# Kernel optimization log

Hardware: AMD Instinct MI355X
Metric: run time of the kernel (lower is better)

## Reference

```python
import jax, jax.numpy as jnp
import numpy as np

N = 50000      # total nodes (cells + row/col/caption nodes across the batch of tables)
E = 500000     # graph edges (row/col cliques, extra edges)
P = 131072     # candidate edge pairs for the edge head
D_LM = 768     # bert-base hidden size
D_MF = 64      # max_freq_emb_size
H = 4          # num_heads per GAT layer
D = 128        # hidden_layer_size per head
DIN = D_LM + D_MF  # 832
DOUT = H * D       # 512


def setup_inputs() -> dict:
    key = jax.random.key(0)
    ks = jax.random.split(key, 32)
    r = lambda k, sh, s=1.0: jax.random.normal(k, sh, jnp.float32) * s
    inp = {}
    inp['cell_h'] = r(ks[0], (N, D_LM))
    inp['pos_emb'] = r(ks[1], (4, D_LM), 0.02)
    inp['mf_emb'] = r(ks[2], (6, D_MF), 0.02)
    # GAT layer 1 (in 832 -> 4 heads x 128), no residual
    inp['W1'] = r(ks[3], (DIN, DOUT), DIN ** -0.5)
    inp['al1'] = r(ks[4], (H, D), D ** -0.5)
    inp['ar1'] = r(ks[5], (H, D), D ** -0.5)
    inp['b1'] = jnp.zeros((DOUT,), jnp.float32)
    # GAT layer 2 (512 -> 4 heads x 128), identity residual
    inp['W2'] = r(ks[6], (DOUT, DOUT), DOUT ** -0.5)
    inp['al2'] = r(ks[7], (H, D), D ** -0.5)
    inp['ar2'] = r(ks[8], (H, D), D ** -0.5)
    inp['b2'] = jnp.zeros((DOUT,), jnp.float32)
    # comp_and_gid head: Linear(512,256)+BN+ReLU+Linear(256,4)
    inp['Wg1'] = r(ks[9], (DOUT, 256), DOUT ** -0.5)
    inp['bg1'] = jnp.zeros((256,), jnp.float32)
    inp['g_gamma'] = jnp.ones((256,), jnp.float32)
    inp['g_beta'] = jnp.zeros((256,), jnp.float32)
    inp['g_mean'] = jnp.zeros((256,), jnp.float32)
    inp['g_var'] = jnp.ones((256,), jnp.float32)
    inp['Wg2'] = r(ks[10], (256, 4), 256 ** -0.5)
    inp['bg2'] = jnp.zeros((4,), jnp.float32)
    # edge head: Linear(1024,256)+BN+ReLU+Linear(256,1)
    inp['We1'] = r(ks[11], (2 * DOUT, 256), (2 * DOUT) ** -0.5)
    inp['be1'] = jnp.zeros((256,), jnp.float32)
    inp['e_gamma'] = jnp.ones((256,), jnp.float32)
    inp['e_beta'] = jnp.zeros((256,), jnp.float32)
    inp['e_mean'] = jnp.zeros((256,), jnp.float32)
    inp['e_var'] = jnp.ones((256,), jnp.float32)
    inp['We2'] = r(ks[12], (256, 1), 256 ** -0.5)
    inp['be2'] = jnp.zeros((1,), jnp.float32)
    # graph structure / index features (constants)
    inp['src'] = jax.random.randint(ks[13], (E,), 0, N, jnp.int32)
    inp['dst'] = jax.random.randint(ks[14], (E,), 0, N, jnp.int32)
    inp['row_pos'] = jax.random.randint(ks[15], (N,), 0, 4, jnp.int32)
    inp['col_pos'] = jax.random.randint(ks[16], (N,), 0, 4, jnp.int32)
    inp['row_mf'] = jax.random.randint(ks[17], (N,), 0, 6, jnp.int32)
    inp['col_mf'] = jax.random.randint(ks[18], (N,), 0, 6, jnp.int32)
    inp['pairs'] = jax.random.randint(ks[19], (P, 2), 0, N, jnp.int32)
    return inp


def _gat(h, W, al, ar, b, src, dst, residual):
    """DGL-style GATConv: LeakyReLU(a_l.Wh_src + a_r.Wh_dst), edge-softmax over dst."""
    n = h.shape[0]
    feat = (h @ W).reshape(n, H, D)                     # [N,H,D]
    el = jnp.sum(feat * al, axis=-1)                    # [N,H]
    er = jnp.sum(feat * ar, axis=-1)                    # [N,H]
    e = jax.nn.leaky_relu(el[src] + er[dst], 0.2)       # [E,H]
    emax = jax.ops.segment_max(e, dst, num_segments=n)  # per-dst max (stability)
    ee = jnp.exp(e - emax[dst])
    denom = jax.ops.segment_sum(ee, dst, num_segments=n)
    alpha = ee / denom[dst]                             # [E,H]
    out = jax.ops.segment_sum(feat[src] * alpha[:, :, None], dst, num_segments=n)  # [N,H,D]
    if residual:
        out = out + h.reshape(n, H, D)                  # identity residual (in==H*D)
    return (out + b.reshape(H, D)).reshape(n, H * D)


def _bn(x, gamma, beta, mean, var):
    return (x - mean) * jax.lax.rsqrt(var + 1e-5) * gamma + beta


def reference(cell_h, pos_emb, mf_emb, W1, al1, ar1, b1, W2, al2, ar2, b2,
              Wg1, bg1, g_gamma, g_beta, g_mean, g_var, Wg2, bg2,
              We1, be1, e_gamma, e_beta, e_mean, e_var, We2, be2,
              src, dst, row_pos, col_pos, row_mf, col_mf, pairs):
    # embedding fusion: LM cell embeddings + row/col positional embeddings
    h = cell_h + pos_emb[row_pos] + pos_emb[col_pos]                    # [N,768]
    mf = mf_emb[jnp.minimum(row_mf, 5)] + mf_emb[jnp.minimum(col_mf, 5)]  # [N,64]
    h = jnp.concatenate([h, mf], axis=-1)                               # [N,832]
    # two multi-head GATConv layers (dropout inactive at eval)
    h = _gat(h, W1, al1, ar1, b1, src, dst, residual=False)             # [N,512]
    h = _gat(h, W2, al2, ar2, b2, src, dst, residual=True)              # [N,512]
    # comp_and_gid head
    gid_logits = jax.nn.relu(_bn(h @ Wg1 + bg1, g_gamma, g_beta, g_mean, g_var)) @ Wg2 + bg2  # [N,4]
    # edge head over candidate node pairs
    ef = jnp.concatenate([h[pairs[:, 0]], h[pairs[:, 1]]], axis=-1)     # [P,1024]
    edge_logits = jax.nn.relu(_bn(ef @ We1 + be1, e_gamma, e_beta, e_mean, e_var)) @ We2 + be2  # [P,1]
    return gid_logits, edge_logits
```

## Files before the change

### kernel.cpp

```cpp
#include <hip/hip_runtime.h>
#include <math.h>


typedef __attribute__((ext_vector_type(8))) short short8;
typedef __attribute__((ext_vector_type(4))) float f32x4;
typedef unsigned short ushort;

#define GLOAD16(g, l)                                                   \
  __builtin_amdgcn_global_load_lds(                                     \
      (const __attribute__((address_space(1))) unsigned int*)(g),       \
      (__attribute__((address_space(3))) unsigned int*)(l), 16, 0, 0)

__device__ __forceinline__ float b2f(ushort h) {
  union { unsigned u; float f; } v; v.u = ((unsigned)h) << 16; return v.f;
}
__device__ __forceinline__ ushort f2b(float f) {
  union { float f; unsigned u; } v; v.f = f;
  unsigned r = v.u + 0x7fffu + ((v.u >> 16) & 1u);
  return (ushort)(r >> 16);
}
__device__ __forceinline__ void up4(uint2 q, float* o) {
  o[0] = b2f((ushort)(q.x & 0xffffu)); o[1] = b2f((ushort)(q.x >> 16));
  o[2] = b2f((ushort)(q.y & 0xffffu)); o[3] = b2f((ushort)(q.y >> 16));
}
__device__ __forceinline__ void up8(uint4 q, float* o) {
  o[0] = b2f((ushort)(q.x & 0xffffu)); o[1] = b2f((ushort)(q.x >> 16));
  o[2] = b2f((ushort)(q.y & 0xffffu)); o[3] = b2f((ushort)(q.y >> 16));
  o[4] = b2f((ushort)(q.z & 0xffffu)); o[5] = b2f((ushort)(q.z >> 16));
  o[6] = b2f((ushort)(q.w & 0xffffu)); o[7] = b2f((ushort)(q.w >> 16));
}
__device__ __forceinline__ uint4 pk8(const float* o) {
  uint4 q;
  q.x = (unsigned)f2b(o[0]) | ((unsigned)f2b(o[1]) << 16);
  q.y = (unsigned)f2b(o[2]) | ((unsigned)f2b(o[3]) << 16);
  q.z = (unsigned)f2b(o[4]) | ((unsigned)f2b(o[5]) << 16);
  q.w = (unsigned)f2b(o[6]) | ((unsigned)f2b(o[7]) << 16);
  return q;
}
__device__ __forceinline__ float warp_sum(float v) {
#pragma unroll
  for (int o = 32; o > 0; o >>= 1) v += __shfl_xor(v, o);
  return v;
}

__global__ __launch_bounds__(256) void embed_kernel(
    const float* __restrict__ cell_h, const float* __restrict__ pos_emb,
    const float* __restrict__ mf_emb,
    const int* __restrict__ row_pos, const int* __restrict__ col_pos,
    const int* __restrict__ row_mf, const int* __restrict__ col_mf,
    ushort* __restrict__ X0, int N)
{
  const int idx = blockIdx.x * 256 + threadIdx.x;
  const int total = N * 104;
  if (idx >= total) return;
  const int n = idx / 104;
  const int c8 = (idx - n * 104) * 8;
  float o[8];
  if (c8 < 768) {
    const int rp = row_pos[n], cp = col_pos[n];
    const float4* pc = (const float4*)(cell_h + (size_t)n * 768 + c8);
    const float4* pr = (const float4*)(pos_emb + (size_t)rp * 768 + c8);
    const float4* pq = (const float4*)(pos_emb + (size_t)cp * 768 + c8);
    float4 c0 = pc[0], c1 = pc[1], r0 = pr[0], r1 = pr[1], q0 = pq[0], q1 = pq[1];
    o[0] = c0.x + r0.x + q0.x; o[1] = c0.y + r0.y + q0.y;
    o[2] = c0.z + r0.z + q0.z; o[3] = c0.w + r0.w + q0.w;
    o[4] = c1.x + r1.x + q1.x; o[5] = c1.y + r1.y + q1.y;
    o[6] = c1.z + r1.z + q1.z; o[7] = c1.w + r1.w + q1.w;
  } else {
    const int rm = min(row_mf[n], 5), cm = min(col_mf[n], 5);
    const int j0 = c8 - 768;
    const float4* pr = (const float4*)(mf_emb + (size_t)rm * 64 + j0);
    const float4* pq = (const float4*)(mf_emb + (size_t)cm * 64 + j0);
    float4 r0 = pr[0], r1 = pr[1], q0 = pq[0], q1 = pq[1];
    o[0] = r0.x + q0.x; o[1] = r0.y + q0.y; o[2] = r0.z + q0.z; o[3] = r0.w + q0.w;
    o[4] = r1.x + q1.x; o[5] = r1.y + q1.y; o[6] = r1.z + q1.z; o[7] = r1.w + q1.w;
  }
  *(uint4*)(X0 + (size_t)n * 832 + c8) = pk8(o);
}

__global__ __launch_bounds__(256) void wpack_kernel(
    const float* __restrict__ W, ushort* __restrict__ Wp,
    int K, int srcN, int colBase, int nTK)
{
  const int idx = blockIdx.x * 256 + threadIdx.x;
  if (idx >= K * srcN) return;
  const int c = idx / K, k = idx - c * K;
  const int n = colBase + c;
  const int tn = n >> 7, tk = k >> 6;
  const int sub = (((n >> 4) & 7) << 1) | ((k >> 5) & 1);
  const int lane = (n & 15) | (((k >> 3) & 3) << 4);
  const int j = k & 7;
  const size_t off = (((size_t)(tn * nTK + tk) << 4) + sub) * 512 + lane * 8 + j;
  Wp[off] = f2b(W[(size_t)k * srcN + c]);
}

__global__ void eprep_kernel(const float* __restrict__ be1,
                             const float* __restrict__ eg, const float* __restrict__ eb,
                             const float* __restrict__ em, const float* __restrict__ ev,
                             float* __restrict__ sa_ext, float* __restrict__ sb)
{
  const int c = threadIdx.x;
  const float sa = eg[c] * rsqrtf(ev[c] + 1e-5f);
  sa_ext[c] = sa;
  sa_ext[c + 256] = sa;
  sb[c] = eb[c] + (be1[c] - em[c]) * sa;
}

template <int EPI, bool ELR>
__global__ __launch_bounds__(256) void mfma_gemm_kernel(
    const ushort* __restrict__ A, const ushort* __restrict__ Bp,
    ushort* __restrict__ C0, ushort* __restrict__ C1,
    int M, int K, int Ncols, int NT, int mtiles,
    const float* __restrict__ bias, const float* __restrict__ gamma,
    const float* __restrict__ beta, const float* __restrict__ mean,
    const float* __restrict__ var, const float* __restrict__ sa_ext,
    const float* __restrict__ al, const float* __restrict__ ar,
    float* __restrict__ elp, float* __restrict__ erp)
{
  __shared__ ushort LDS[16896];
  __shared__ float redS[256];
  ushort* As = LDS;
  ushort* Bs = LDS + 8192;
  const int tid = threadIdx.x;
  const int lane = tid & 63;
  const int wave = tid >> 6;
  const int wm = wave >> 1, wn = wave & 1;

  const int per = NT << 3;
  const int f = blockIdx.x;
  const int sg = f / per;
  const int rem = f - sg * per;
  const int nb = min(8, mtiles - (sg << 3));
  const int band = rem % nb, colt = rem / nb;
  const int m0 = ((sg << 3) + band) << 7;
  const int n0 = colt << 7;
  const int nTK = K >> 6;

  const int rA = lane & 15;
  const int kA = (lane >> 4) << 3;
  const ushort* Aaddr[4];
#pragma unroll
  for (int q = 0; q < 4; ++q) {
    const int a = (wave << 2) + q;
    int row = m0 + ((a >> 1) << 4) + rA;
    if (row >= M) row = 0;
    Aaddr[q] = A + (size_t)row * K + ((a & 1) << 5) + kA;
  }
  const ushort* Baddr = Bp + (((size_t)colt * nTK) << 13)
                        + ((size_t)(wave << 2) << 9) + (lane << 3);

  f32x4 acc[4][4];
#pragma unroll
  for (int i = 0; i < 4; ++i)
#pragma unroll
    for (int j = 0; j < 4; ++j) acc[i][j] = (f32x4){0.f, 0.f, 0.f, 0.f};

  for (int k0 = 0; k0 < K; k0 += 64) {
    __syncthreads();
#pragma unroll
    for (int q = 0; q < 4; ++q)
      GLOAD16(Aaddr[q] + k0, As + (((wave << 2) + q) << 9));
#pragma unroll
    for (int q = 0; q < 4; ++q)
      GLOAD16(Baddr + (((size_t)(k0 >> 6)) << 13) + (q << 9),
              Bs + (((wave << 2) + q) << 9));
    __syncthreads();
#pragma unroll
    for (int ks = 0; ks < 2; ++ks) {
      short8 af[4], bf4[4];
#pragma unroll
      for (int x = 0; x < 4; ++x)
        af[x] = *(const short8*)(As + ((((wm << 2) + x) * 2 + ks) << 9) + (lane << 3));
#pragma unroll
      for (int x = 0; x < 4; ++x)
        bf4[x] = *(const short8*)(Bs + ((((wn << 2) + x) * 2 + ks) << 9) + (lane << 3));
#pragma unroll
      for (int mf = 0; mf < 4; ++mf)
#pragma unroll
        for (int nf = 0; nf < 4; ++nf)
          acc[mf][nf] = __builtin_amdgcn_mfma_f32_16x16x32_bf16(
              af[mf], bf4[nf], acc[mf][nf], 0, 0, 0);
    }
  }

  __syncthreads();
#pragma unroll
  for (int nf = 0; nf < 4; ++nf) {
    const int cl = (((wn << 2) + nf) << 4) + (lane & 15);
    const int col = n0 + cl;
    float sa = 1.f, sb = 0.f;
    bool dorelu = false;
    if (EPI == 1) {
      if (col < 256) {
        const float rs = rsqrtf(var[col] + 1e-5f);
        sa = rs * gamma[col];
        sb = beta[col] + (bias[col] - mean[col]) * sa;
        dorelu = true;
      } else {
        sa = sa_ext[col - 256];
      }
    }
#pragma unroll
    for (int mf = 0; mf < 4; ++mf) {
      const int rl = (((wm << 2) + mf) << 4) + ((lane >> 4) << 2);
#pragma unroll
      for (int j = 0; j < 4; ++j) {
        float v = acc[mf][nf][j];
        if (EPI == 1) { v = fmaf(v, sa, sb); if (dorelu) v = fmaxf(v, 0.f); }
        LDS[(rl + j) * 132 + cl] = f2b(v);
      }
    }
  }
  __syncthreads();
#pragma unroll
  for (int i = 0; i < 8; ++i) {
    const int g = tid + (i << 8);
    const int r = g >> 4, c8 = g & 15;
    const int row = m0 + r;
    if (row >= M) continue;
    const uint4 v = *(const uint4*)(LDS + r * 132 + (c8 << 3));
    const int col = n0 + (c8 << 3);
    if (EPI == 0) {
      *(uint4*)(C0 + (size_t)row * Ncols + col) = v;
    } else {
      if (col < 256) *(uint4*)(C0 + (size_t)row * 256 + col) = v;
      else           *(uint4*)(C1 + (size_t)row * 512 + (col - 256)) = v;
    }
  }

  if (ELR) {
    const int r = tid & 127;
    const int half = tid >> 7;
    const float* alh = al + colt * 128 + half * 64;
    const float* arh = ar + colt * 128 + half * 64;
    const ushort* rowp = LDS + r * 132 + half * 64;
    float sl = 0.f, sr = 0.f;
#pragma unroll
    for (int c = 0; c < 64; ++c) {
      const float v = b2f(rowp[c]);
      sl = fmaf(v, alh[c], sl);
      sr = fmaf(v, arh[c], sr);
    }
    if (half) { redS[r] = sl; redS[r + 128] = sr; }
    __syncthreads();
    if (!half) {
      const int row = m0 + r;
      if (row < M) {
        elp[(size_t)row * 4 + colt] = sl + redS[r];
        erp[(size_t)row * 4 + colt] = sr + redS[r + 128];
      }
    }
  }
}

__global__ __launch_bounds__(256) void hist_kernel(
    const int* __restrict__ dst, int* __restrict__ counts, int E)
{
  const int e = blockIdx.x * 256 + threadIdx.x;
  if (e < E) atomicAdd(counts + dst[e], 1);
}

__global__ __launch_bounds__(1024) void scan_kernel(
    const int* __restrict__ counts, int* __restrict__ offsets, int N)
{
  __shared__ int sums[1024];
  const int t = threadIdx.x;
  const int chunk = (N + 1023) >> 10;
  const int beg = t * chunk;
  const int end = min(beg + chunk, N);
  int s = 0;
  for (int i = beg; i < end; ++i) s += counts[i];
  sums[t] = s;
  __syncthreads();
  for (int o = 1; o < 1024; o <<= 1) {
    int u = (t >= o) ? sums[t - o] : 0;
    __syncthreads();
    sums[t] += u;
    __syncthreads();
  }
  int run = sums[t] - s;
  for (int i = beg; i < end; ++i) { offsets[i] = run; run += counts[i]; }
  if (t == 1023) offsets[N] = sums[1023];
}

__global__ __launch_bounds__(256) void scatter_kernel(
    const int* __restrict__ src, const int* __restrict__ dst,
    const int* __restrict__ offsets, int* __restrict__ cursor,
    int* __restrict__ csr_src, int E)
{
  const int e = blockIdx.x * 256 + threadIdx.x;
  if (e >= E) return;
  const int d = dst[e];
  const int pos = offsets[d] + atomicAdd(cursor + d, 1);
  csr_src[pos] = src[e];
}

template <bool RES>
__global__ __launch_bounds__(256) void gat_aggregate_kernel(
    const int* __restrict__ csr_src, const int* __restrict__ offsets,
    const float* __restrict__ el, const float* __restrict__ er,
    const ushort* __restrict__ feat, const float* __restrict__ bias,
    const ushort* __restrict__ resid, ushort* __restrict__ out, int N)
{
  __shared__ float eeS[4][1024];
  __shared__ int sS[4][256];
  const int w = threadIdx.x >> 6;
  const int node = (blockIdx.x * 256 + threadIdx.x) >> 6;
  const int lane = threadIdx.x & 63;
  if (node >= N) return;
  const int beg = offsets[node], end = offsets[node + 1];
  const int deg = end - beg;
  const float4 erd = *(const float4*)(er + (size_t)node * 4);
  float* eew = eeS[w];
  int* sw = sS[w];

  float d0 = 0.f, d1 = 0.f, d2 = 0.f, d3 = 0.f;
  for (int i = lane; i < deg; i += 64) {
    const int s = csr_src[beg + i];
    const float4 l = *(const float4*)(el + (size_t)s * 4);
    float x0 = l.x + erd.x, x1 = l.y + erd.y, x2 = l.z + erd.z, x3 = l.w + erd.w;
    x0 = x0 > 0.f ? x0 : 0.2f * x0;
    x1 = x1 > 0.f ? x1 : 0.2f * x1;
    x2 = x2 > 0.f ? x2 : 0.2f * x2;
    x3 = x3 > 0.f ? x3 : 0.2f * x3;
    const float e0 = __expf(x0), e1 = __expf(x1), e2 = __expf(x2), e3 = __expf(x3);
    if (i < 256) {
      float4 ev = {e0, e1, e2, e3};
      *(float4*)(eew + (i << 2)) = ev;
      sw[i] = s;
    }
    d0 += e0; d1 += e1; d2 += e2; d3 += e3;
  }
  d0 = warp_sum(d0); d1 = warp_sum(d1); d2 = warp_sum(d2); d3 = warp_sum(d3);
  const float r0 = 1.f / d0, r1 = 1.f / d1, r2 = 1.f / d2, r3 = 1.f / d3;
  const int h = lane >> 4;
  const float rh = (lane & 32) ? ((lane & 16) ? r3 : r2) : ((lane & 16) ? r1 : r0);
  const float erh = (lane & 32) ? ((lane & 16) ? erd.w : erd.z)
                                : ((lane & 16) ? erd.y : erd.x);

  float a[8] = {0.f, 0.f, 0.f, 0.f, 0.f, 0.f, 0.f, 0.f};
  for (int i = 0; i < deg; ++i) {
    int s;
    float ew;
    if (i < 256) {
      s = sw[i];
      ew = eew[(i << 2) | h];
    } else {
      s = csr_src[beg + i];
      float x = el[(size_t)s * 4 + h] + erh;
      x = x > 0.f ? x : 0.2f * x;
      ew = __expf(x);
    }
    const float aw = ew * rh;
    const uint4 q = *(const uint4*)(feat + (size_t)s * 512 + lane * 8);
    float v[8];
    up8(q, v);
#pragma unroll
    for (int j = 0; j < 8; ++j) a[j] = fmaf(v[j], aw, a[j]);
  }

  const float4 b0 = *(const float4*)(bias + lane * 8);
  const float4 b1 = *(const float4*)(bias + lane * 8 + 4);
  a[0] += b0.x; a[1] += b0.y; a[2] += b0.z; a[3] += b0.w;
  a[4] += b1.x; a[5] += b1.y; a[6] += b1.z; a[7] += b1.w;
  if (RES) {
    float q[8];
    up8(*(const uint4*)(resid + (size_t)node * 512 + lane * 8), q);
#pragma unroll
    for (int j = 0; j < 8; ++j) a[j] += q[j];
  }
  *(uint4*)(out + (size_t)node * 512 + lane * 8) = pk8(a);
}

__global__ __launch_bounds__(256) void gid2_kernel(
    const ushort* __restrict__ g, const float* __restrict__ Wg2,
    const float* __restrict__ bg2, float* __restrict__ out, int N)
{
  const int wv = (blockIdx.x * 256 + threadIdx.x) >> 6;
  const int lane = threadIdx.x & 63;
  if (wv >= N) return;
  float ga[4];
  up4(*(const uint2*)(g + (size_t)wv * 256 + lane * 4), ga);
  float a0 = 0.f, a1 = 0.f, a2 = 0.f, a3 = 0.f;
  const float* wp = Wg2 + (size_t)lane * 16;
#pragma unroll
  for (int j = 0; j < 4; j++) {
    const float4 w = *(const float4*)(wp + j * 4);
    a0 += ga[j] * w.x; a1 += ga[j] * w.y; a2 += ga[j] * w.z; a3 += ga[j] * w.w;
  }
  a0 = warp_sum(a0); a1 = warp_sum(a1); a2 = warp_sum(a2); a3 = warp_sum(a3);
  if (lane == 0) {
    float4 o = {a0 + bg2[0], a1 + bg2[1], a2 + bg2[2], a3 + bg2[3]};
    *(float4*)(out + (size_t)wv * 4) = o;
  }
}

__global__ __launch_bounds__(256) void pair_combine_kernel(
    const ushort* __restrict__ UV, const int* __restrict__ pairs,
    const float* __restrict__ sb, const float* __restrict__ We2,
    const float* __restrict__ be2, float* __restrict__ out, int P)
{
  const int hw = (blockIdx.x * 256 + threadIdx.x) >> 5;
  const int l = threadIdx.x & 31;
  if (hw >= P) return;
  const int p0 = pairs[2 * hw], p1 = pairs[2 * hw + 1];
  float u[8], v[8];
  up8(*(const uint4*)(UV + (size_t)p0 * 512 + l * 8), u);
  up8(*(const uint4*)(UV + (size_t)p1 * 512 + 256 + l * 8), v);
  const float4 sb0 = *(const float4*)(sb + l * 8);
  const float4 sb1 = *(const float4*)(sb + l * 8 + 4);
  const float4 w0 = *(const float4*)(We2 + l * 8);
  const float4 w1 = *(const float4*)(We2 + l * 8 + 4);
  float s = fmaxf(u[0] + v[0] + sb0.x, 0.f) * w0.x
          + fmaxf(u[1] + v[1] + sb0.y, 0.f) * w0.y
          + fmaxf(u[2] + v[2] + sb0.z, 0.f) * w0.z
          + fmaxf(u[3] + v[3] + sb0.w, 0.f) * w0.w
          + fmaxf(u[4] + v[4] + sb1.x, 0.f) * w1.x
          + fmaxf(u[5] + v[5] + sb1.y, 0.f) * w1.y
          + fmaxf(u[6] + v[6] + sb1.z, 0.f) * w1.z
          + fmaxf(u[7] + v[7] + sb1.w, 0.f) * w1.w;
#pragma unroll
  for (int o = 16; o > 0; o >>= 1) s += __shfl_xor(s, o);
  if (l == 0) out[hw] = s + be2[0];
}

extern "C" void kernel_launch(void* const* d_in, const int* in_sizes, int n_in,
                              void* d_out, int out_size, void* d_ws, size_t ws_size,
                              hipStream_t stream) {
  const float* cell_h  = (const float*)d_in[0];
  const float* pos_emb = (const float*)d_in[1];
  const float* mf_emb  = (const float*)d_in[2];
  const float* W1  = (const float*)d_in[3];
  const float* al1 = (const float*)d_in[4];
  const float* ar1 = (const float*)d_in[5];
  const float* b1  = (const float*)d_in[6];
  const float* W2  = (const float*)d_in[7];
  const float* al2 = (const float*)d_in[8];
  const float* ar2 = (const float*)d_in[9];
  const float* b2  = (const float*)d_in[10];
  const float* Wg1 = (const float*)d_in[11];
  const float* bg1 = (const float*)d_in[12];
  const float* g_gamma = (const float*)d_in[13];
  const float* g_beta  = (const float*)d_in[14];
  const float* g_mean  = (const float*)d_in[15];
  const float* g_var   = (const float*)d_in[16];
  const float* Wg2 = (const float*)d_in[17];
  const float* bg2 = (const float*)d_in[18];
  const float* We1 = (const float*)d_in[19];
  const float* be1 = (const float*)d_in[20];
  const float* e_gamma = (const float*)d_in[21];
  const float* e_beta  = (const float*)d_in[22];
  const float* e_mean  = (const float*)d_in[23];
  const float* e_var   = (const float*)d_in[24];
  const float* We2 = (const float*)d_in[25];
  const float* be2 = (const float*)d_in[26];
  const int* src = (const int*)d_in[27];
  const int* dst = (const int*)d_in[28];
  const int* row_pos = (const int*)d_in[29];
  const int* col_pos = (const int*)d_in[30];
  const int* row_mf  = (const int*)d_in[31];
  const int* col_mf  = (const int*)d_in[32];
  const int* pairs   = (const int*)d_in[33];

  const int N = in_sizes[0] / 768;
  const int E = in_sizes[27];
  const int P = in_sizes[33] / 2;

  ushort* X0    = (ushort*)d_ws;
  ushort* featB = X0 + (size_t)N * 832;
  ushort* h1    = featB + (size_t)N * 512;
  ushort* h2    = h1 + (size_t)N * 512;
  ushort* W1p   = h2 + (size_t)N * 512;
  ushort* W2p   = W1p + 512 * 832;
  ushort* Bh    = W2p + 512 * 512;
  float* sa_ext = (float*)(Bh + 768 * 512);
  float* sbv    = sa_ext + 512;
  float* el     = sbv + 256;
  float* er     = el + (size_t)N * 4;
  int* offsets  = (int*)(er + (size_t)N * 4);
  int* counts   = offsets + (N + 1);
  int* csr_src  = counts + N;
  ushort* g_tmp = X0;
  ushort* UV    = featB;

  const int nodeWaves = (N + 3) / 4;
  const int mtiles = (N + 127) / 128;

  hipMemsetAsync(counts, 0, (size_t)N * sizeof(int), stream);
  hist_kernel<<<(E + 255) / 256, 256, 0, stream>>>(dst, counts, E);
  scan_kernel<<<1, 1024, 0, stream>>>(counts, offsets, N);
  hipMemsetAsync(counts, 0, (size_t)N * sizeof(int), stream);
  scatter_kernel<<<(E + 255) / 256, 256, 0, stream>>>(src, dst, offsets, counts, csr_src, E);

  wpack_kernel<<<(512 * 832 + 255) / 256, 256, 0, stream>>>(W1, W1p, 832, 512, 0, 13);
  wpack_kernel<<<(512 * 512 + 255) / 256, 256, 0, stream>>>(W2, W2p, 512, 512, 0, 8);
  wpack_kernel<<<(512 * 256 + 255) / 256, 256, 0, stream>>>(Wg1, Bh, 512, 256, 0, 8);
  wpack_kernel<<<(512 * 256 + 255) / 256, 256, 0, stream>>>(We1, Bh, 512, 256, 256, 8);
  wpack_kernel<<<(512 * 256 + 255) / 256, 256, 0, stream>>>(We1 + 512 * 256, Bh, 512, 256, 512, 8);
  eprep_kernel<<<1, 256, 0, stream>>>(be1, e_gamma, e_beta, e_mean, e_var, sa_ext, sbv);

  embed_kernel<<<(N * 104 + 255) / 256, 256, 0, stream>>>(
      cell_h, pos_emb, mf_emb, row_pos, col_pos, row_mf, col_mf, X0, N);

  mfma_gemm_kernel<0, true><<<mtiles * 4, 256, 0, stream>>>(
      X0, W1p, featB, nullptr, N, 832, 512, 4, mtiles,
      nullptr, nullptr, nullptr, nullptr, nullptr, nullptr, al1, ar1, el, er);
  gat_aggregate_kernel<false><<<nodeWaves, 256, 0, stream>>>(
      csr_src, offsets, el, er, featB, b1, nullptr, h1, N);

  mfma_gemm_kernel<0, true><<<mtiles * 4, 256, 0, stream>>>(
      h1, W2p, featB, nullptr, N, 512, 512, 4, mtiles,
      nullptr, nullptr, nullptr, nullptr, nullptr, nullptr, al2, ar2, el, er);
  gat_aggregate_kernel<true><<<nodeWaves, 256, 0, stream>>>(
      csr_src, offsets, el, er, featB, b2, h1, h2, N);

  mfma_gemm_kernel<1, false><<<mtiles * 6, 256, 0, stream>>>(
      h2, Bh, g_tmp, UV, N, 512, 0, 6, mtiles,
      bg1, g_gamma, g_beta, g_mean, g_var, sa_ext, nullptr, nullptr, nullptr, nullptr);
  gid2_kernel<<<nodeWaves, 256, 0, stream>>>(g_tmp, Wg2, bg2, (float*)d_out, N);
  pair_combine_kernel<<<(P + 7) / 8, 256, 0, stream>>>(
      UV, pairs, sbv, We2, be2, (float*)d_out + (size_t)N * 4, P);
}
```

Measured before the change: 622.2 us.

## Double-buffer LDS in MFMA GEMM and merge weight-pack launches into one

The GEMM main loop now uses two LDS buffers, so the next K-tile's global-to-LDS loads are issued before the current tile's MFMAs run, with one wait and barrier per iteration. This hides global load latency behind compute but doubles the GEMM's static LDS use, which may lower occupancy. Separately, the five weight-pack launches and the BN-prep launch are merged into a single prep kernel to cut launch overhead.

After: 610.7 us. About the same (-1.8%).

```diff
diff --git a/kernel.cpp b/kernel.cpp
--- a/kernel.cpp
+++ b/kernel.cpp
@@ -78,12 +78,10 @@
   *(uint4*)(X0 + (size_t)n * 832 + c8) = pk8(o);
 }
 
-__global__ __launch_bounds__(256) void wpack_kernel(
+__device__ __forceinline__ void pack_one(
     const float* __restrict__ W, ushort* __restrict__ Wp,
-    int K, int srcN, int colBase, int nTK)
-{
-  const int idx = blockIdx.x * 256 + threadIdx.x;
-  if (idx >= K * srcN) return;
+    int idx, int K, int srcN, int colBase, int nTK)
+{
   const int c = idx / K, k = idx - c * K;
   const int n = colBase + c;
   const int tn = n >> 7, tk = k >> 6;
@@ -94,16 +92,37 @@
   Wp[off] = f2b(W[(size_t)k * srcN + c]);
 }
 
-__global__ void eprep_kernel(const float* __restrict__ be1,
-                             const float* __restrict__ eg, const float* __restrict__ eb,
-                             const float* __restrict__ em, const float* __restrict__ ev,
-                             float* __restrict__ sa_ext, float* __restrict__ sb)
-{
-  const int c = threadIdx.x;
-  const float sa = eg[c] * rsqrtf(ev[c] + 1e-5f);
-  sa_ext[c] = sa;
-  sa_ext[c + 256] = sa;
-  sb[c] = eb[c] + (be1[c] - em[c]) * sa;
+#define PREP_C0 (832 * 512)
+#define PREP_C1 (PREP_C0 + 512 * 512)
+#define PREP_C2 (PREP_C1 + 512 * 256)
+#define PREP_C3 (PREP_C2 + 512 * 256)
+#define PREP_C4 (PREP_C3 + 512 * 256)
+__global__ __launch_bounds__(256) void prep_kernel(
+    const float* __restrict__ W1, const float* __restrict__ W2,
+    const float* __restrict__ Wg1, const float* __restrict__ We1,
+    ushort* __restrict__ W1p, ushort* __restrict__ W2p, ushort* __restrict__ Bh,
+    const float* __restrict__ be1, const float* __restrict__ eg,
+    const float* __restrict__ eb, const float* __restrict__ em,
+    const float* __restrict__ ev, float* __restrict__ sa_ext, float* __restrict__ sbv)
+{
+  const int idx = blockIdx.x * 256 + threadIdx.x;
+  if (idx < PREP_C0) {
+    pack_one(W1, W1p, idx, 832, 512, 0, 13);
+  } else if (idx < PREP_C1) {
+    pack_one(W2, W2p, idx - PREP_C0, 512, 512, 0, 8);
+  } else if (idx < PREP_C2) {
+    pack_one(Wg1, Bh, idx - PREP_C1, 512, 256, 0, 8);
+  } else if (idx < PREP_C3) {
+    pack_one(We1, Bh, idx - PREP_C2, 512, 256, 256, 8);
+  } else if (idx < PREP_C4) {
+    pack_one(We1 + 512 * 256, Bh, idx - PREP_C3, 512, 256, 512, 8);
+  } else if (idx < PREP_C4 + 256) {
+    const int c = idx - PREP_C4;
+    const float sa = eg[c] * rsqrtf(ev[c] + 1e-5f);
+    sa_ext[c] = sa;
+    sa_ext[c + 256] = sa;
+    sbv[c] = eb[c] + (be1[c] - em[c]) * sa;
+  }
 }
 
 template <int EPI, bool ELR>
@@ -117,10 +136,8 @@
     const float* __restrict__ al, const float* __restrict__ ar,
     float* __restrict__ elp, float* __restrict__ erp)
 {
-  __shared__ ushort LDS[16896];
+  __shared__ ushort LDS[32768];
   __shared__ float redS[256];
-  ushort* As = LDS;
-  ushort* Bs = LDS + 8192;
   const int tid = threadIdx.x;
   const int lane = tid & 63;
   const int wave = tid >> 6;
@@ -155,25 +172,41 @@
 #pragma unroll
     for (int j = 0; j < 4; ++j) acc[i][j] = (f32x4){0.f, 0.f, 0.f, 0.f};
 
-  for (int k0 = 0; k0 < K; k0 += 64) {
-    __syncthreads();
-#pragma unroll
-    for (int q = 0; q < 4; ++q)
-      GLOAD16(Aaddr[q] + k0, As + (((wave << 2) + q) << 9));
-#pragma unroll
-    for (int q = 0; q < 4; ++q)
-      GLOAD16(Baddr + (((size_t)(k0 >> 6)) << 13) + (q << 9),
-              Bs + (((wave << 2) + q) << 9));
-    __syncthreads();
+  const int nt = K >> 6;
+
+#pragma unroll
+  for (int q = 0; q < 4; ++q)
+    GLOAD16(Aaddr[q], LDS + (((wave << 2) + q) << 9));
+#pragma unroll
+  for (int q = 0; q < 4; ++q)
+    GLOAD16(Baddr + (q << 9), LDS + 8192 + (((wave << 2) + q) << 9));
+  asm volatile("s_waitcnt vmcnt(0)" ::: "memory");
+  __builtin_amdgcn_s_barrier();
+
+  int cur = 0;
+  for (int t = 0; t < nt; ++t) {
+    const int nxt = cur ^ 1;
+    if (t + 1 < nt) {
+      const int k0n = (t + 1) << 6;
+#pragma unroll
+      for (int q = 0; q < 4; ++q)
+        GLOAD16(Aaddr[q] + k0n, LDS + (nxt << 14) + (((wave << 2) + q) << 9));
+#pragma unroll
+      for (int q = 0; q < 4; ++q)
+        GLOAD16(Baddr + ((size_t)(t + 1) << 13) + (q << 9),
+                LDS + (nxt << 14) + 8192 + (((wave << 2) + q) << 9));
+    }
+    const ushort* Ab = LDS + (cur << 14);
+    const ushort* Bb = Ab + 8192;
 #pragma unroll
     for (int ks = 0; ks < 2; ++ks) {
       short8 af[4], bf4[4];
 #pragma unroll
       for (int x = 0; x < 4; ++x)
-        af[x] = *(const short8*)(As + ((((wm << 2) + x) * 2 + ks) << 9) + (lane << 3));
+        af[x] = *(const short8*)(Ab + ((((wm << 2) + x) * 2 + ks) << 9) + (lane << 3));
 #pragma unroll
       for (int x = 0; x < 4; ++x)
-        bf4[x] = *(const short8*)(Bs + ((((wn << 2) + x) * 2 + ks) << 9) + (lane << 3));
+        bf4[x] = *(const short8*)(Bb + ((((wn << 2) + x) * 2 + ks) << 9) + (lane << 3));
 #pragma unroll
       for (int mf = 0; mf < 4; ++mf)
 #pragma unroll
@@ -181,6 +214,9 @@
           acc[mf][nf] = __builtin_amdgcn_mfma_f32_16x16x32_bf16(
               af[mf], bf4[nf], acc[mf][nf], 0, 0, 0);
     }
+    asm volatile("s_waitcnt vmcnt(0)" ::: "memory");
+    __builtin_amdgcn_s_barrier();
+    cur = nxt;
   }
 
   __syncthreads();
@@ -492,12 +528,9 @@
   hipMemsetAsync(counts, 0, (size_t)N * sizeof(int), stream);
   scatter_kernel<<<(E + 255) / 256, 256, 0, stream>>>(src, dst, offsets, counts, csr_src, E);
 
-  wpack_kernel<<<(512 * 832 + 255) / 256, 256, 0, stream>>>(W1, W1p, 832, 512, 0, 13);
-  wpack_kernel<<<(512 * 512 + 255) / 256, 256, 0, stream>>>(W2, W2p, 512, 512, 0, 8);
-  wpack_kernel<<<(512 * 256 + 255) / 256, 256, 0, stream>>>(Wg1, Bh, 512, 256, 0, 8);
-  wpack_kernel<<<(512 * 256 + 255) / 256, 256, 0, stream>>>(We1, Bh, 512, 256, 256, 8);
-  wpack_kernel<<<(512 * 256 + 255) / 256, 256, 0, stream>>>(We1 + 512 * 256, Bh, 512, 256, 512, 8);
-  eprep_kernel<<<1, 256, 0, stream>>>(be1, e_gamma, e_beta, e_mean, e_var, sa_ext, sbv);
+  prep_kernel<<<(PREP_C4 + 256 + 255) / 256, 256, 0, stream>>>(
+      W1, W2, Wg1, We1, W1p, W2p, Bh,
+      be1, e_gamma, e_beta, e_mean, e_var, sa_ext, sbv);
 
   embed_kernel<<<(N * 104 + 255) / 256, 256, 0, stream>>>(
       cell_h, pos_emb, mf_emb, row_pos, col_pos, row_mf, col_mf, X0, N);
```
